# Kernel optimization log

Hardware: AMD Instinct MI355X
Metric: run time of the kernel (lower is better)

## Reference

```python
import jax, jax.numpy as jnp
import numpy as np

B, H, W, CIN, C, L = 2, 512, 512, 64, 64, 4
TAU = 1.0


def _conv3x3(x, w):
    # NHWC input, HWIO kernel, SAME zero padding, stride 1 (SignalConv2D corr=True)
    return jax.lax.conv_general_dilated(
        x, w, window_strides=(1, 1), padding='SAME',
        dimension_numbers=('NHWC', 'HWIO', 'NHWC'))


def setup_inputs() -> dict:
    key = jax.random.key(0)
    ks = jax.random.split(key, 10)
    return {
        'x0': jax.random.normal(ks[0], (B, H, W, CIN), jnp.float32),
        'spa_mask': jax.random.uniform(ks[1], (B, H, W, 1), jnp.float32),
        'gumbel_u': jax.random.uniform(ks[2], (1, L, 2, C), jnp.float32),
        'ch_mask': jax.random.uniform(ks[3], (1, L, 2, C), jnp.float32),
        'w0': jax.random.normal(ks[4], (3, 3, CIN, C), jnp.float32) * 0.05,
        'w1': jax.random.normal(ks[5], (3, 3, C, C), jnp.float32) * 0.05,
        'w2': jax.random.normal(ks[6], (3, 3, C, C), jnp.float32) * 0.05,
        'w3': jax.random.normal(ks[7], (3, 3, C, C), jnp.float32) * 0.05,
        'w_collect': jax.random.normal(ks[8], (L * C, C), jnp.float32) * 0.05,
        'b_collect': jnp.zeros((C,), jnp.float32),
    }


def reference(x0, spa_mask, gumbel_u, ch_mask, w0, w1, w2, w3, w_collect, b_collect):
    # Gumbel-softmax channel routing mask over the {dense, sparse} axis (axis=2)
    g = -jnp.log(-jnp.log(jnp.clip(gumbel_u, 1e-10, 1.0)))
    ch = jax.nn.softmax((ch_mask + g) / TAU, axis=2)  # (1, L, 2, C)

    ws = [w0, w1, w2, w3]
    out_feats = []
    fea = x0
    for i in range(L):
        cd = ch[:, i, 0, :][:, None, None, :]  # dense-channel mask  (1,1,1,C)
        cs = ch[:, i, 1, :][:, None, None, :]  # sparse-channel mask (1,1,1,C)
        if i == 0:
            fea = _conv3x3(fea, ws[0])
            fea = fea * cs * spa_mask + fea * cd
        else:
            cdp = ch[:, i - 1, 0, :][:, None, None, :]
            csp = ch[:, i - 1, 1, :][:, None, None, :]
            fea_d = _conv3x3(fea * cdp, ws[i])
            fea_s = _conv3x3(fea * csp, ws[i])
            fea = (fea_d * cs * spa_mask + fea_d * cd
                   + fea_s * cs * spa_mask + fea_s * cd * spa_mask)
        fea = jax.nn.relu(fea)
        out_feats.append(fea)

    cat = jnp.concatenate(out_feats, axis=-1)  # (B, H, W, L*C)
    # 1x1 stride-1 Conv2DTranspose == pointwise linear + bias
    out = jnp.einsum('bhwi,io->bhwo', cat, w_collect) + b_collect
    return out, ch
```

## Files before the change

### kernel.cpp

```cpp
#include <hip/hip_runtime.h>
#include <hip/hip_fp16.h>

#define BB 2
#define HH 512
#define WW 512
#define CC 64
#define PW 514

typedef _Float16 f16;
typedef _Float16 f16x8 __attribute__((ext_vector_type(8)));
typedef float f32x4 __attribute__((ext_vector_type(4)));

static __device__ __forceinline__ f16x8 zero_f16x8() {
    f16x8 z = {(f16)0,(f16)0,(f16)0,(f16)0,(f16)0,(f16)0,(f16)0,(f16)0};
    return z;
}

static __device__ __forceinline__ f16x8 cvt_pair(f32x4 a, f32x4 b) {
    f16x8 o;
    o[0]=(f16)a[0]; o[1]=(f16)a[1]; o[2]=(f16)a[2]; o[3]=(f16)a[3];
    o[4]=(f16)b[0]; o[5]=(f16)b[1]; o[6]=(f16)b[2]; o[7]=(f16)b[3];
    return o;
}

__global__ void k_prep_ch(const float* __restrict__ gum, const float* __restrict__ chm,
                          float* __restrict__ ws_ch, float* __restrict__ out_ch) {
    int t = threadIdx.x;
    int l = t >> 6, c = t & 63;
    float u0 = gum[(l*2+0)*64+c], u1 = gum[(l*2+1)*64+c];
    u0 = fminf(fmaxf(u0, 1e-10f), 1.0f);
    u1 = fminf(fmaxf(u1, 1e-10f), 1.0f);
    float a0 = chm[(l*2+0)*64+c] - logf(-logf(u0));
    float a1 = chm[(l*2+1)*64+c] - logf(-logf(u1));
    float m = fmaxf(a0, a1);
    float e0 = expf(a0-m), e1 = expf(a1-m);
    float s = e0 + e1;
    float c0 = e0/s, c1 = e1/s;
    ws_ch[(l*2+0)*64+c] = c0;  ws_ch[(l*2+1)*64+c] = c1;
    out_ch[(l*2+0)*64+c] = c0; out_ch[(l*2+1)*64+c] = c1;
}

__global__ void k_pack(const float* __restrict__ w0, const float* __restrict__ w1,
                       const float* __restrict__ w2, const float* __restrict__ w3,
                       const float* __restrict__ wc, const float* __restrict__ ch,
                       f16* __restrict__ bpk0, f16* __restrict__ bpkL, f16* __restrict__ wcpk) {
    int idx = blockIdx.x * 256 + threadIdx.x;
    if (idx < 36864) {
        int j = idx & 7, lane = (idx>>3)&63, nb = (idx>>9)&3, kb = idx>>11;
        int k = kb*32 + (lane>>4)*8 + j;
        int tap = k>>6, ci = k&63;
        int co = nb*16 + (lane&15);
        bpk0[idx] = (f16)w0[(tap*64+ci)*64+co];
    } else if (idx < 36864 + 221184) {
        int i2 = idx - 36864;
        int l = i2 / 73728;
        int r = i2 % 73728;
        int j = r&7, lane=(r>>3)&63, nb=(r>>9)&7, kb=r>>12;
        int k = kb*32 + (lane>>4)*8 + j;
        int tap = k>>6, ci = k&63;
        int copr = nb*16 + (lane&15);
        int co = copr & 63;
        const float* w = (l==0)? w1 : (l==1)? w2 : w3;
        float scale = (copr < 64) ? ch[(l*2+0)*64+ci] : ch[(l*2+1)*64+ci];
        bpkL[i2] = (f16)(w[(tap*64+ci)*64+co] * scale);
    } else if (idx < 36864 + 221184 + 16384) {
        int i3 = idx - (36864 + 221184);
        int j=i3&7, lane=(i3>>3)&63, nb=(i3>>9)&3, kb=(i3>>11)&1, l=i3>>12;
        int k = kb*32 + (lane>>4)*8 + j;
        int n = nb*16 + (lane&15);
        wcpk[i3] = (f16)wc[(l*64+k)*64+n];
    }
}

__global__ void k_guard(f16* __restrict__ buf) {
    int idx = blockIdx.x*256 + threadIdx.x;
    const int TOT = 2*2052*8;
    if (idx >= TOT) return;
    int c8 = idx & 7, g = idx >> 3;
    int b = g / 2052, r = g % 2052;
    int hp, wp;
    if      (r < 514)  { hp = 0;        wp = r; }
    else if (r < 1028) { hp = 513;      wp = r-514; }
    else if (r < 1540) { hp = r-1027;   wp = 0; }
    else               { hp = r-1539;   wp = 513; }
    *(f16x8*)(buf + ((size_t)(b*PW+hp)*PW + wp)*64 + c8*8) = zero_f16x8();
}

template<int MODE>
__global__ __launch_bounds__(256, 3) void k_conv(const void* __restrict__ in_, f16* __restrict__ out,
        const f16* __restrict__ bpk, const float* __restrict__ ch_l,
        const float* __restrict__ spa) {
    constexpr int NBT = (MODE==0) ? 4 : 8;
    constexpr int NF  = (MODE==0) ? 1 : 2;
    __shared__ f16 smem[3*136*64];
    const int wt = blockIdx.x, h = blockIdx.y, b = blockIdx.z;
    const int tid = threadIdx.x, lane = tid & 63, wid = tid >> 6;
    const int px0 = wt*128;
    const int sub  = lane & 7;
    const int srel = lane >> 3;
    const int cblk = sub ^ srel;

    const float* inF = (const float*)in_;

    f32x4 v0c[5], v1c[5];
    bool okc[5];
    int dstc[5];

    if (MODE == 0) {
        {
            f32x4 v0[9], v1[9];
            bool ok[9];
            int dst[9];
            #pragma unroll
            for (int t = 0; t < 9; ++t) {
                int j = t*4 + wid;
                ok[t] = false;
                if (j < 34) {
                    int r = j / 17, i = j % 17;
                    int s = i*8 + srel;
                    int hin = h + r - 1, win = px0 + s - 1;
                    ok[t] = ((unsigned)hin < HH) && ((unsigned)win < WW);
                    dst[t] = r*17408 + i*1024 + lane*16;
                    if (ok[t]) {
                        const f32x4* p = (const f32x4*)(inF + (((size_t)(b*HH + hin)*WW + win)*CC + cblk*8));
                        v0[t] = p[0];
                        v1[t] = p[1];
                    }
                }
            }
            #pragma unroll
            for (int t = 0; t < 9; ++t) {
                if (t*4 + wid < 34) {
                    f16x8 o = ok[t] ? cvt_pair(v0[t], v1[t]) : zero_f16x8();
                    *(f16x8*)((char*)smem + dst[t]) = o;
                }
            }
        }
        __syncthreads();
        #pragma unroll
        for (int t = 0; t < 5; ++t) {
            int i = t*4 + wid;
            okc[t] = false;
            if (i < 17) {
                int s = i*8 + srel;
                int hin = h + 1, win = px0 + s - 1;
                okc[t] = ((unsigned)hin < HH) && ((unsigned)win < WW);
                dstc[t] = 2*17408 + i*1024 + lane*16;
                if (okc[t]) {
                    const f32x4* p = (const f32x4*)(inF + (((size_t)(b*HH + hin)*WW + win)*CC + cblk*8));
                    v0c[t] = p[0];
                    v1c[t] = p[1];
                }
            }
        }
        __builtin_amdgcn_sched_barrier(0);
    } else {
        const f16* inH = (const f16*)in_;
        #pragma unroll
        for (int jj = 0; jj < 9; ++jj) {
            int j = jj*4 + wid;
            if (j < 34) {
                int r = j / 17, i = j % 17;
                int s = i*8 + srel;
                const f16* src = inH + ((size_t)(b*PW + h + r)*PW + (px0 + s))*64 + cblk*8;
                __builtin_amdgcn_global_load_lds(
                    (const __attribute__((address_space(1))) uint32_t*)src,
                    (__attribute__((address_space(3))) uint32_t*)
                        ((char*)smem + r*17408 + i*1024),
                    16, 0, 0);
            }
        }
        __syncthreads();
        #pragma unroll
        for (int t = 0; t < 5; ++t) {
            int i = t*4 + wid;
            if (i < 17) {
                int s = i*8 + srel;
                const f16* src = inH + ((size_t)(b*PW + h + 2)*PW + (px0 + s))*64 + cblk*8;
                __builtin_amdgcn_global_load_lds(
                    (const __attribute__((address_space(1))) uint32_t*)src,
                    (__attribute__((address_space(3))) uint32_t*)
                        ((char*)smem + 2*17408 + i*1024),
                    16, 0, 0);
            }
        }
    }

    const int wn = wid;
    const int lrow = lane & 15, q = lane >> 4;

    int sb0[8], po[2][3];
    #pragma unroll
    for (int dxi = 0; dxi < 3; ++dxi) {
        int m7 = (lrow + dxi) & 7;
        po[0][dxi] = ((q)     ^ m7) * 16;
        po[1][dxi] = ((4 + q) ^ m7) * 16;
    }
    #pragma unroll
    for (int mf = 0; mf < 8; ++mf)
        sb0[mf] = (mf*16 + lrow) * 128;

    f32x4 acc[8][NF];
    #pragma unroll
    for (int i=0;i<8;i++)
        #pragma unroll
        for (int j=0;j<NF;j++) { f32x4 z = {0.f,0.f,0.f,0.f}; acc[i][j] = z; }

    int nbIdx[2];
    nbIdx[0] = wn; nbIdx[1] = wn + 4;

    const f16* blane = bpk + (size_t)lane*8;

    f16x8 acur[8], bcur[NF], bnxt[NF];
    #pragma unroll
    for (int nf=0; nf<NF; ++nf)
        bcur[nf] = *reinterpret_cast<const f16x8*>(blane + (size_t)nbIdx[nf]*512);

    #pragma unroll
    for (int kb = 0; kb < 18; ++kb) {
        if (kb == 11) {
            if (MODE == 0) {
                #pragma unroll
                for (int t = 0; t < 5; ++t) {
                    if (t*4 + wid < 17) {
                        f16x8 o = okc[t] ? cvt_pair(v0c[t], v1c[t]) : zero_f16x8();
                        *(f16x8*)((char*)smem + dstc[t]) = o;
                    }
                }
            }
            __syncthreads();
        }
        const int rn = kb/6, dxi = (kb%6)/2, half = kb & 1;
        #pragma unroll
        for (int mf=0; mf<8; ++mf)
            acur[mf] = *(const f16x8*)((const char*)smem + rn*17408 + sb0[mf] + dxi*128 + po[half][dxi]);
        if (kb < 17) {
            const int kn = kb + 1;
            #pragma unroll
            for (int nf=0; nf<NF; ++nf)
                bnxt[nf] = *reinterpret_cast<const f16x8*>(blane + (size_t)(kn*NBT + nbIdx[nf])*512);
        }
        __builtin_amdgcn_s_setprio(1);
        #pragma unroll
        for (int nf=0; nf<NF; ++nf) {
            #pragma unroll
            for (int mf=0; mf<8; ++mf)
                acc[mf][nf] = __builtin_amdgcn_mfma_f32_16x16x32_f16(acur[mf], bcur[nf], acc[mf][nf], 0,0,0);
        }
        __builtin_amdgcn_s_setprio(0);
        #pragma unroll
        for (int nf=0; nf<NF; ++nf) bcur[nf] = bnxt[nf];
    }

    const float* cd = ch_l;
    const float* cs = ch_l + 64;
    const size_t sparow = (size_t)(b*HH + h)*WW;
    const size_t outrow = (size_t)(b*PW + h + 1)*PW + 1;
    const int co = wn*16 + lrow;
    const float vcd = cd[co], vcs = cs[co];
    #pragma unroll
    for (int mf=0; mf<8; ++mf) {
        const int pixb = mf*16 + q*4;
        f32x4 sp4 = *(const f32x4*)(spa + sparow + px0 + pixb);
        #pragma unroll
        for (int r=0; r<4; ++r) {
            float sp = sp4[r];
            float v;
            if (MODE==0) v = acc[mf][0][r] * (vcs*sp + vcd);
            else         v = acc[mf][0][r] * (vcs*sp + vcd) + acc[mf][1][r] * sp;
            v = fmaxf(v, 0.f);
            out[(outrow + px0 + pixb + r)*64 + co] = (f16)v;
        }
    }
}

__global__ __launch_bounds__(256) void k_collect_all(
        const f16* __restrict__ f0, const f16* __restrict__ f1,
        const f16* __restrict__ f2, const f16* __restrict__ f3,
        const f16* __restrict__ wcpk, const float* __restrict__ bias,
        float* __restrict__ out) {
    const int wt = blockIdx.x, h = blockIdx.y, b = blockIdx.z;
    const int tid = threadIdx.x;
    const int lane = tid & 63, wid = tid >> 6;
    const int lrow = lane & 15, lk = (lane>>4)*8;
    const size_t inrow  = (size_t)(b*PW + h + 1)*PW + 1;
    const size_t outrow = (size_t)(b*HH + h)*WW;
    const int px0 = wt*256 + wid*64;

    const f16* feas[4] = {f0, f1, f2, f3};

    f32x4 acc[4][4];
    #pragma unroll
    for (int i=0;i<4;i++)
        #pragma unroll
        for (int j=0;j<4;j++) { f32x4 z = {0.f,0.f,0.f,0.f}; acc[i][j] = z; }

    f16x8 a_cur[4], a_nxt[4];
    #pragma unroll
    for (int mf=0; mf<4; ++mf)
        a_cur[mf] = *reinterpret_cast<const f16x8*>(f0 + (inrow + px0 + mf*16 + lrow)*64 + lk);

    #pragma unroll
    for (int kb=0; kb<8; ++kb) {
        if (kb < 7) {
            const f16* fl = feas[(kb+1)>>1];
            #pragma unroll
            for (int mf=0; mf<4; ++mf)
                a_nxt[mf] = *reinterpret_cast<const f16x8*>(fl + (inrow + px0 + mf*16 + lrow)*64 + ((kb+1)&1)*32 + lk);
        }
        #pragma unroll
        for (int nf=0; nf<4; ++nf) {
            f16x8 bb = *reinterpret_cast<const f16x8*>(wcpk + ((size_t)(kb*4 + nf)*64 + lane)*8);
            #pragma unroll
            for (int mf=0; mf<4; ++mf)
                acc[mf][nf] = __builtin_amdgcn_mfma_f32_16x16x32_f16(bb, a_cur[mf], acc[mf][nf], 0,0,0);
        }
        #pragma unroll
        for (int mf=0; mf<4; ++mf) a_cur[mf] = a_nxt[mf];
    }
    const int q = lane >> 4;
    #pragma unroll
    for (int mf=0; mf<4; ++mf) {
        const int pix = px0 + mf*16 + lrow;
        float* orow = out + (outrow + pix)*CC;
        #pragma unroll
        for (int nf=0; nf<4; ++nf) {
            const int co0 = nf*16 + q*4;
            f32x4 b4 = *(const f32x4*)(bias + co0);
            *(f32x4*)(orow + co0) = acc[mf][nf] + b4;
        }
    }
}

template<bool FIRST>
__global__ __launch_bounds__(256) void k_collect(const f16* __restrict__ fea,
        const f16* __restrict__ wcpk_l, const float* __restrict__ bias,
        float* __restrict__ out) {
    const int wt = blockIdx.x, h = blockIdx.y, b = blockIdx.z;
    const int tid = threadIdx.x;
    const int lane = tid & 63, wid = tid >> 6;
    const int lrow = lane & 15, lk = (lane>>4)*8;
    const size_t inrow  = (size_t)(b*PW + h + 1)*PW + 1;
    const size_t outrow = (size_t)(b*HH + h)*WW;
    const int px0 = wt*64 + wid*16;

    f32x4 acc[4];
    #pragma unroll
    for (int j=0;j<4;j++) { f32x4 z = {0.f,0.f,0.f,0.f}; acc[j] = z; }

    #pragma unroll
    for (int kb=0; kb<2; ++kb) {
        f16x8 a = *reinterpret_cast<const f16x8*>(fea + (inrow + px0 + lrow)*64 + kb*32 + lk);
        #pragma unroll
        for (int nf=0; nf<4; ++nf) {
            f16x8 bb = *reinterpret_cast<const f16x8*>(wcpk_l + ((size_t)(kb*4 + nf)*64 + lane)*8);
            acc[nf] = __builtin_amdgcn_mfma_f32_16x16x32_f16(bb, a, acc[nf], 0,0,0);
        }
    }
    const int q = lane >> 4;
    const int pix = px0 + lrow;
    float* orow = out + (outrow + pix)*CC;
    #pragma unroll
    for (int nf=0; nf<4; ++nf) {
        const int co0 = nf*16 + q*4;
        f32x4 v = acc[nf];
        #pragma unroll
        for (int r=0;r<4;++r) {
            float x = v[r];
            if (FIRST) x += bias[co0+r];
            else       x += orow[co0+r];
            orow[co0+r] = x;
        }
    }
}

extern "C" void kernel_launch(void* const* d_in, const int* in_sizes, int n_in,
                              void* d_out, int out_size, void* d_ws, size_t ws_size,
                              hipStream_t stream) {
    const float* x0  = (const float*)d_in[0];
    const float* spa = (const float*)d_in[1];
    const float* gum = (const float*)d_in[2];
    const float* chm = (const float*)d_in[3];
    const float* w0  = (const float*)d_in[4];
    const float* w1  = (const float*)d_in[5];
    const float* w2  = (const float*)d_in[6];
    const float* w3  = (const float*)d_in[7];
    const float* wc  = (const float*)d_in[8];
    const float* bias= (const float*)d_in[9];
    float* out = (float*)d_out;

    char* ws = (char*)d_ws;
    const size_t WBASE = (1u<<20);
    const size_t FB = 67699712ull;
    const size_t NEED_A = WBASE + 4*FB;
    const size_t NEED_B = WBASE + 2*FB;
    if (ws_size < NEED_B) return;

    float* ws_ch = (float*)ws;
    f16* bpk0 = (f16*)(ws + 4096);
    f16* bpkL = (f16*)(ws + 4096 + 73728);
    f16* wcpk = (f16*)(ws + 4096 + 73728 + 442368);

    k_prep_ch<<<1, 256, 0, stream>>>(gum, chm, ws_ch, out + 33554432);
    k_pack<<<1072, 256, 0, stream>>>(w0, w1, w2, w3, wc, ws_ch, bpk0, bpkL, wcpk);

    dim3 gcv(4, 512, 2);
    dim3 gca(2, 512, 2);
    dim3 gcf(8, 512, 2);

    if (ws_size >= NEED_A) {
        f16* R0 = (f16*)(ws + WBASE);
        f16* R1 = (f16*)(ws + WBASE + FB);
        f16* R2 = (f16*)(ws + WBASE + 2*FB);
        f16* R3 = (f16*)(ws + WBASE + 3*FB);
        k_guard<<<129, 256, 0, stream>>>(R1);
        k_guard<<<129, 256, 0, stream>>>(R2);
        k_guard<<<129, 256, 0, stream>>>(R3);
        k_conv<0><<<gcv, 256, 0, stream>>>(x0, R1, bpk0,          ws_ch + 0,   spa);
        k_conv<1><<<gcv, 256, 0, stream>>>(R1, R2, bpkL + 0,      ws_ch + 128, spa);
        k_conv<1><<<gcv, 256, 0, stream>>>(R2, R3, bpkL + 73728,  ws_ch + 256, spa);
        k_conv<1><<<gcv, 256, 0, stream>>>(R3, R0, bpkL + 147456, ws_ch + 384, spa);
        k_collect_all<<<gca, 256, 0, stream>>>(R1, R2, R3, R0, wcpk, bias, out);
    } else {
        f16* P0 = (f16*)(ws + WBASE);
        f16* P1 = (f16*)(ws + WBASE + FB);
        k_guard<<<129, 256, 0, stream>>>(P0);
        k_guard<<<129, 256, 0, stream>>>(P1);
        k_conv<0><<<gcv, 256, 0, stream>>>(x0, P1, bpk0,          ws_ch + 0,   spa);
        k_collect<true ><<<gcf, 256, 0, stream>>>(P1, wcpk + 0,     bias, out);
        k_conv<1><<<gcv, 256, 0, stream>>>(P1, P0, bpkL + 0,      ws_ch + 128, spa);
        k_collect<false><<<gcf, 256, 0, stream>>>(P0, wcpk + 4096,  bias, out);
        k_conv<1><<<gcv, 256, 0, stream>>>(P0, P1, bpkL + 73728,  ws_ch + 256, spa);
        k_collect<false><<<gcf, 256, 0, stream>>>(P1, wcpk + 8192,  bias, out);
        k_conv<1><<<gcv, 256, 0, stream>>>(P1, P0, bpkL + 147456, ws_ch + 384, spa);
        k_collect<false><<<gcf, 256, 0, stream>>>(P0, wcpk + 12288, bias, out);
    }
}
```

Measured before the change: 364.0 us.

## Process eight output rows per conv block with rolling four-slot LDS row buffer

Each conv block now loops over eight consecutive output rows and keeps a rotating four-row ring of input rows in shared memory. Each step loads only one new row, so the two halo rows are no longer re-read for every output row. The warps are retiled into a 2x2 layout (64 pixels by 32 channels each) in place of 128 pixels by 16 channels. This raises per-wave accumulator count and lowers the occupancy target from 3 to 2. It also reduces the grid by a factor of eight, which may leave fewer blocks in flight to hide latency.

```diff
diff --git a/kernel.cpp b/kernel.cpp
--- a/kernel.cpp
+++ b/kernel.cpp
@@ -6,6 +6,7 @@
 #define WW 512
 #define CC 64
 #define PW 514
+#define ROWS 8
 
 typedef _Float16 f16;
 typedef _Float16 f16x8 __attribute__((ext_vector_type(8)));
@@ -87,13 +88,15 @@
 }
 
 template<int MODE>
-__global__ __launch_bounds__(256, 3) void k_conv(const void* __restrict__ in_, f16* __restrict__ out,
+__global__ __launch_bounds__(256, 2) void k_conv(const void* __restrict__ in_, f16* __restrict__ out,
         const f16* __restrict__ bpk, const float* __restrict__ ch_l,
         const float* __restrict__ spa) {
     constexpr int NBT = (MODE==0) ? 4 : 8;
-    constexpr int NF  = (MODE==0) ? 1 : 2;
-    __shared__ f16 smem[3*136*64];
-    const int wt = blockIdx.x, h = blockIdx.y, b = blockIdx.z;
+    constexpr int NF  = (MODE==0) ? 2 : 4;
+    __shared__ f16 smem[4*136*64];
+    char* smb = (char*)smem;
+    const int wt = blockIdx.x, by = blockIdx.y, b = blockIdx.z;
+    const int h0 = by*ROWS;
     const int tid = threadIdx.x, lane = tid & 63, wid = tid >> 6;
     const int px0 = wt*128;
     const int sub  = lane & 7;
@@ -101,175 +104,192 @@
     const int cblk = sub ^ srel;
 
     const float* inF = (const float*)in_;
-
-    f32x4 v0c[5], v1c[5];
-    bool okc[5];
-    int dstc[5];
+    const f16*   inH = (const f16*)in_;
+
+    f32x4 pv0[5], pv1[5];
+    bool pok[5];
+    int pdst[5];
 
     if (MODE == 0) {
-        {
-            f32x4 v0[9], v1[9];
-            bool ok[9];
-            int dst[9];
-            #pragma unroll
-            for (int t = 0; t < 9; ++t) {
-                int j = t*4 + wid;
-                ok[t] = false;
-                if (j < 34) {
-                    int r = j / 17, i = j % 17;
-                    int s = i*8 + srel;
-                    int hin = h + r - 1, win = px0 + s - 1;
-                    ok[t] = ((unsigned)hin < HH) && ((unsigned)win < WW);
-                    dst[t] = r*17408 + i*1024 + lane*16;
-                    if (ok[t]) {
-                        const f32x4* p = (const f32x4*)(inF + (((size_t)(b*HH + hin)*WW + win)*CC + cblk*8));
-                        v0[t] = p[0];
-                        v1[t] = p[1];
+        #pragma unroll
+        for (int r = 0; r < 3; ++r) {
+            const int p = h0 + r;
+            const int hin = p - 1;
+            #pragma unroll
+            for (int t = 0; t < 5; ++t) {
+                int i2 = t*4 + wid;
+                pok[t] = false;
+                if (i2 < 17) {
+                    int s = i2*8 + srel;
+                    int win = px0 + s - 1;
+                    pok[t] = ((unsigned)hin < HH) && ((unsigned)win < WW);
+                    pdst[t] = (p&3)*17408 + i2*1024 + lane*16;
+                    if (pok[t]) {
+                        const f32x4* pp = (const f32x4*)(inF + (((size_t)(b*HH + hin)*WW + win)*CC + cblk*8));
+                        pv0[t] = pp[0];
+                        pv1[t] = pp[1];
                     }
                 }
             }
             #pragma unroll
-            for (int t = 0; t < 9; ++t) {
-                if (t*4 + wid < 34) {
-                    f16x8 o = ok[t] ? cvt_pair(v0[t], v1[t]) : zero_f16x8();
-                    *(f16x8*)((char*)smem + dst[t]) = o;
-                }
-            }
-        }
-        __syncthreads();
-        #pragma unroll
-        for (int t = 0; t < 5; ++t) {
-            int i = t*4 + wid;
-            okc[t] = false;
-            if (i < 17) {
-                int s = i*8 + srel;
-                int hin = h + 1, win = px0 + s - 1;
-                okc[t] = ((unsigned)hin < HH) && ((unsigned)win < WW);
-                dstc[t] = 2*17408 + i*1024 + lane*16;
-                if (okc[t]) {
-                    const f32x4* p = (const f32x4*)(inF + (((size_t)(b*HH + hin)*WW + win)*CC + cblk*8));
-                    v0c[t] = p[0];
-                    v1c[t] = p[1];
-                }
-            }
-        }
-        __builtin_amdgcn_sched_barrier(0);
+            for (int t = 0; t < 5; ++t) {
+                if (t*4 + wid < 17) {
+                    f16x8 o = pok[t] ? cvt_pair(pv0[t], pv1[t]) : zero_f16x8();
+                    *(f16x8*)(smb + pdst[t]) = o;
+                }
+            }
+        }
     } else {
-        const f16* inH = (const f16*)in_;
-        #pragma unroll
-        for (int jj = 0; jj < 9; ++jj) {
-            int j = jj*4 + wid;
-            if (j < 34) {
-                int r = j / 17, i = j % 17;
-                int s = i*8 + srel;
-                const f16* src = inH + ((size_t)(b*PW + h + r)*PW + (px0 + s))*64 + cblk*8;
-                __builtin_amdgcn_global_load_lds(
-                    (const __attribute__((address_space(1))) uint32_t*)src,
-                    (__attribute__((address_space(3))) uint32_t*)
-                        ((char*)smem + r*17408 + i*1024),
-                    16, 0, 0);
-            }
-        }
-        __syncthreads();
-        #pragma unroll
-        for (int t = 0; t < 5; ++t) {
-            int i = t*4 + wid;
-            if (i < 17) {
-                int s = i*8 + srel;
-                const f16* src = inH + ((size_t)(b*PW + h + 2)*PW + (px0 + s))*64 + cblk*8;
-                __builtin_amdgcn_global_load_lds(
-                    (const __attribute__((address_space(1))) uint32_t*)src,
-                    (__attribute__((address_space(3))) uint32_t*)
-                        ((char*)smem + 2*17408 + i*1024),
-                    16, 0, 0);
-            }
-        }
-    }
-
-    const int wn = wid;
+        #pragma unroll
+        for (int r = 0; r < 3; ++r) {
+            const int p = h0 + r;
+            #pragma unroll
+            for (int t = 0; t < 5; ++t) {
+                int i2 = t*4 + wid;
+                if (i2 < 17) {
+                    int s = i2*8 + srel;
+                    const f16* src = inH + ((size_t)(b*PW + p)*PW + (px0 + s))*64 + cblk*8;
+                    __builtin_amdgcn_global_load_lds(
+                        (const __attribute__((address_space(1))) uint32_t*)src,
+                        (__attribute__((address_space(3))) uint32_t*)
+                            (smb + (p&3)*17408 + i2*1024),
+                        16, 0, 0);
+                }
+            }
+        }
+    }
+
+    const int wm = wid >> 1, wn = wid & 1;
     const int lrow = lane & 15, q = lane >> 4;
 
-    int sb0[8], po[2][3];
+    int sb[4][3], po[2][3];
     #pragma unroll
     for (int dxi = 0; dxi < 3; ++dxi) {
         int m7 = (lrow + dxi) & 7;
         po[0][dxi] = ((q)     ^ m7) * 16;
         po[1][dxi] = ((4 + q) ^ m7) * 16;
-    }
-    #pragma unroll
-    for (int mf = 0; mf < 8; ++mf)
-        sb0[mf] = (mf*16 + lrow) * 128;
-
-    f32x4 acc[8][NF];
-    #pragma unroll
-    for (int i=0;i<8;i++)
-        #pragma unroll
-        for (int j=0;j<NF;j++) { f32x4 z = {0.f,0.f,0.f,0.f}; acc[i][j] = z; }
-
-    int nbIdx[2];
-    nbIdx[0] = wn; nbIdx[1] = wn + 4;
-
+        #pragma unroll
+        for (int mf = 0; mf < 4; ++mf)
+            sb[mf][dxi] = (wm*64 + mf*16 + lrow + dxi) * 128;
+    }
+
+    int nbIdx[4];
+    nbIdx[0]=wn*2; nbIdx[1]=wn*2+1; nbIdx[2]=wn*2+4; nbIdx[3]=wn*2+5;
     const f16* blane = bpk + (size_t)lane*8;
 
-    f16x8 acur[8], bcur[NF], bnxt[NF];
-    #pragma unroll
-    for (int nf=0; nf<NF; ++nf)
-        bcur[nf] = *reinterpret_cast<const f16x8*>(blane + (size_t)nbIdx[nf]*512);
-
-    #pragma unroll
-    for (int kb = 0; kb < 18; ++kb) {
-        if (kb == 11) {
+    const float* cd = ch_l;
+    const float* cs = ch_l + 64;
+
+    for (int i = 0; i < ROWS; ++i) {
+        __syncthreads();
+
+        if (i < ROWS-1) {
+            const int p = h0 + i + 3;
             if (MODE == 0) {
+                const int hin = p - 1;
                 #pragma unroll
                 for (int t = 0; t < 5; ++t) {
-                    if (t*4 + wid < 17) {
-                        f16x8 o = okc[t] ? cvt_pair(v0c[t], v1c[t]) : zero_f16x8();
-                        *(f16x8*)((char*)smem + dstc[t]) = o;
+                    int i2 = t*4 + wid;
+                    pok[t] = false;
+                    if (i2 < 17) {
+                        int s = i2*8 + srel;
+                        int win = px0 + s - 1;
+                        pok[t] = (hin < HH) && ((unsigned)win < WW);
+                        pdst[t] = (p&3)*17408 + i2*1024 + lane*16;
+                        if (pok[t]) {
+                            const f32x4* pp = (const f32x4*)(inF + (((size_t)(b*HH + hin)*WW + win)*CC + cblk*8));
+                            pv0[t] = pp[0];
+                            pv1[t] = pp[1];
+                        }
                     }
                 }
-            }
-            __syncthreads();
-        }
-        const int rn = kb/6, dxi = (kb%6)/2, half = kb & 1;
-        #pragma unroll
-        for (int mf=0; mf<8; ++mf)
-            acur[mf] = *(const f16x8*)((const char*)smem + rn*17408 + sb0[mf] + dxi*128 + po[half][dxi]);
-        if (kb < 17) {
-            const int kn = kb + 1;
-            #pragma unroll
-            for (int nf=0; nf<NF; ++nf)
-                bnxt[nf] = *reinterpret_cast<const f16x8*>(blane + (size_t)(kn*NBT + nbIdx[nf])*512);
-        }
-        __builtin_amdgcn_s_setprio(1);
-        #pragma unroll
-        for (int nf=0; nf<NF; ++nf) {
-            #pragma unroll
-            for (int mf=0; mf<8; ++mf)
-                acc[mf][nf] = __builtin_amdgcn_mfma_f32_16x16x32_f16(acur[mf], bcur[nf], acc[mf][nf], 0,0,0);
-        }
-        __builtin_amdgcn_s_setprio(0);
-        #pragma unroll
-        for (int nf=0; nf<NF; ++nf) bcur[nf] = bnxt[nf];
-    }
-
-    const float* cd = ch_l;
-    const float* cs = ch_l + 64;
-    const size_t sparow = (size_t)(b*HH + h)*WW;
-    const size_t outrow = (size_t)(b*PW + h + 1)*PW + 1;
-    const int co = wn*16 + lrow;
-    const float vcd = cd[co], vcs = cs[co];
-    #pragma unroll
-    for (int mf=0; mf<8; ++mf) {
-        const int pixb = mf*16 + q*4;
-        f32x4 sp4 = *(const f32x4*)(spa + sparow + px0 + pixb);
-        #pragma unroll
-        for (int r=0; r<4; ++r) {
-            float sp = sp4[r];
-            float v;
-            if (MODE==0) v = acc[mf][0][r] * (vcs*sp + vcd);
-            else         v = acc[mf][0][r] * (vcs*sp + vcd) + acc[mf][1][r] * sp;
-            v = fmaxf(v, 0.f);
-            out[(outrow + px0 + pixb + r)*64 + co] = (f16)v;
+                __builtin_amdgcn_sched_barrier(0);
+            } else {
+                #pragma unroll
+                for (int t = 0; t < 5; ++t) {
+                    int i2 = t*4 + wid;
+                    if (i2 < 17) {
+                        int s = i2*8 + srel;
+                        const f16* src = inH + ((size_t)(b*PW + p)*PW + (px0 + s))*64 + cblk*8;
+                        __builtin_amdgcn_global_load_lds(
+                            (const __attribute__((address_space(1))) uint32_t*)src,
+                            (__attribute__((address_space(3))) uint32_t*)
+                                (smb + (p&3)*17408 + i2*1024),
+                            16, 0, 0);
+                    }
+                }
+            }
+        }
+
+        f32x4 acc[4][NF];
+        #pragma unroll
+        for (int m=0;m<4;m++)
+            #pragma unroll
+            for (int j=0;j<NF;j++) { f32x4 z = {0.f,0.f,0.f,0.f}; acc[m][j] = z; }
+
+        f16x8 acur[4], bcur[NF], bnxt[NF];
+        #pragma unroll
+        for (int nf=0; nf<NF; ++nf)
+            bcur[nf] = *reinterpret_cast<const f16x8*>(blane + (size_t)nbIdx[nf]*512);
+
+        #pragma unroll
+        for (int kb = 0; kb < 18; ++kb) {
+            const int rn = kb/6, dxi = (kb%6)/2, half = kb & 1;
+            const int slot = (i + rn) & 3;
+            #pragma unroll
+            for (int mf=0; mf<4; ++mf)
+                acur[mf] = *(const f16x8*)(smb + slot*17408 + sb[mf][dxi] + po[half][dxi]);
+            if (kb < 17) {
+                const int kn = kb + 1;
+                #pragma unroll
+                for (int nf=0; nf<NF; ++nf)
+                    bnxt[nf] = *reinterpret_cast<const f16x8*>(blane + (size_t)(kn*NBT + nbIdx[nf])*512);
+            }
+            __builtin_amdgcn_s_setprio(1);
+            #pragma unroll
+            for (int nf=0; nf<NF; ++nf) {
+                #pragma unroll
+                for (int mf=0; mf<4; ++mf)
+                    acc[mf][nf] = __builtin_amdgcn_mfma_f32_16x16x32_f16(acur[mf], bcur[nf], acc[mf][nf], 0,0,0);
+            }
+            __builtin_amdgcn_s_setprio(0);
+            #pragma unroll
+            for (int nf=0; nf<NF; ++nf) bcur[nf] = bnxt[nf];
+        }
+
+        {
+            const int h = h0 + i;
+            const size_t sparow = (size_t)(b*HH + h)*WW;
+            const size_t outrow = (size_t)(b*PW + h + 1)*PW + 1;
+            #pragma unroll
+            for (int mf=0; mf<4; ++mf) {
+                const int pixb = wm*64 + mf*16 + q*4;
+                f32x4 sp4 = *(const f32x4*)(spa + sparow + px0 + pixb);
+                #pragma unroll
+                for (int nf2=0; nf2<2; ++nf2) {
+                    int co = wn*32 + nf2*16 + lrow;
+                    float vcd = cd[co], vcs = cs[co];
+                    #pragma unroll
+                    for (int r=0; r<4; ++r) {
+                        float sp = sp4[r];
+                        float v;
+                        if (MODE==0) v = acc[mf][nf2][r] * (vcs*sp + vcd);
+                        else         v = acc[mf][nf2][r] * (vcs*sp + vcd) + acc[mf][nf2+2][r] * sp;
+                        v = fmaxf(v, 0.f);
+                        out[(outrow + px0 + pixb + r)*64 + co] = (f16)v;
+                    }
+                }
+            }
+        }
+
+        if (MODE == 0 && i < ROWS-1) {
+            #pragma unroll
+            for (int t = 0; t < 5; ++t) {
+                if (t*4 + wid < 17) {
+                    f16x8 o = pok[t] ? cvt_pair(pv0[t], pv1[t]) : zero_f16x8();
+                    *(f16x8*)(smb + pdst[t]) = o;
+                }
+            }
         }
     }
 }
@@ -404,7 +424,7 @@
     k_prep_ch<<<1, 256, 0, stream>>>(gum, chm, ws_ch, out + 33554432);
     k_pack<<<1072, 256, 0, stream>>>(w0, w1, w2, w3, wc, ws_ch, bpk0, bpkL, wcpk);
 
-    dim3 gcv(4, 512, 2);
+    dim3 gcv(4, 512/ROWS, 2);
     dim3 gca(2, 512, 2);
     dim3 gcf(8, 512, 2);
 
```

New measurement: 848.0 us. +133.0%, slower.
